# Kernel optimization log

Measured on AMD Instinct MI355X. Metric: run time of the kernel, lower is better.

## Reference

```python
import jax, jax.numpy as jnp
import numpy as np

MARGIN = 0.5        # contrastive margin (init kwarg)
NUM_LABELS = 20     # label ids are in [0, NUM_LABELS)


def setup_inputs() -> dict:
    key = jax.random.key(0)
    k1, k2 = jax.random.split(key)
    emb = jax.random.normal(k1, (4, 16, 64, 64), dtype=jnp.float32)
    lab = jax.random.randint(k2, (4, 64, 64), 0, NUM_LABELS, dtype=jnp.int32)
    return {"emb": emb, "lab": lab}


def _loss_one(x, y):
    # x: (C, H, W) embedding, y: (H, W) int labels
    C, H, W = x.shape
    N = H * W
    xf = x.reshape(C, N)
    # per-pixel centering across channels, then L2-normalize across channels
    xc = xf - jnp.mean(xf, axis=0, keepdims=True)
    nrm = jnp.sqrt(jnp.sum(xc * xc, axis=0))           # (N,)
    denom = jnp.where(nrm > 0, nrm, 1.0)
    e = jnp.where(nrm > 0, xc / denom, 0.0).T          # (N, C); NaN-mask -> 0
    sim = (e @ e.T) * 0.5 + 0.5                        # (N, N) in [0, 1]

    yi = y.reshape(N)
    yf = yi.astype(jnp.float32) + 1.0
    eq = yf[:, None] == yf[None, :]
    nz = (yf[:, None] * yf[None, :]) != 0.0            # product-zero exclusion (faithful)
    lp = jnp.where(nz, jnp.where(eq, 1.0, -1.0), 0.0)  # label-pair matrix

    # inverse-frequency per-pixel weights, outer product for pairs
    cnt = jnp.zeros((NUM_LABELS,), jnp.float32).at[yi].add(1.0)
    wpix = 1.0 / cnt[yi]                               # (N,)
    Wm = wpix[:, None] * wpix[None, :]                 # (N, N)

    # positive pairs: relu(1 - sim); negative pairs: relu(sim - margin)
    loss = jnp.where(lp == 1.0, jnp.maximum(1.0 - sim, 0.0),
                     jnp.where(lp == -1.0, jnp.maximum(sim - MARGIN, 0.0), 0.0))
    return jnp.sum(Wm * loss) / N


def reference(emb, lab):
    return jnp.sum(jax.vmap(_loss_one)(emb, lab))
```

## Files before the change

kernel.cpp:

```cpp
#include <hip/hip_runtime.h>

#define NUM_LABELS 20
#define N_PIX 4096
#define C_DIM 16
#define BATCH 4

#define PTILE 128
#define PNT (N_PIX / PTILE)
#define PTPAIRS (PNT * (PNT + 1) / 2)
#define NPAIRS (BATCH * PTPAIRS)
#define NBLK 704
#define BLK_PER_BATCH 176
#define KPAD 24

typedef __attribute__((ext_vector_type(8))) short bf16x8;
typedef __attribute__((ext_vector_type(4))) float f32x4;

__device__ __forceinline__ unsigned int bf16rne(float f) {
    unsigned int x = __float_as_uint(f);
    return (x + 0x7fffu + ((x >> 16) & 1u)) >> 16;
}

__global__ __launch_bounds__(256) void pair_kernel(
    const float* __restrict__ emb,
    const int*   __restrict__ lab,
    float* __restrict__ partials)
{
    const int bk   = blockIdx.x;
    const int b    = bk / BLK_PER_BATCH;
    const int t    = threadIdx.x;
    const int lane = t & 63;
    const int wv   = t >> 6;

    __shared__ int   h[NUM_LABELS];
    __shared__ float rinv[NUM_LABELS];
    __shared__ unsigned short sI[PTILE * KPAD];
    __shared__ unsigned short sJ[PTILE * KPAD];
    __shared__ int   syI[PTILE], syJ[PTILE];
    __shared__ float wred[4];

    if (t < NUM_LABELS) h[t] = 0;
    __syncthreads();
    {
        const int* yb = lab + (size_t)b * N_PIX;
        int cnt[NUM_LABELS];
#pragma unroll
        for (int l = 0; l < NUM_LABELS; ++l) cnt[l] = 0;
        for (int it = 0; it < 16; ++it) {
            const int y = yb[wv * 1024 + it * 64 + lane];
#pragma unroll
            for (int l = 0; l < NUM_LABELS; ++l)
                cnt[l] += (int)__popcll(__ballot(y == l));
        }
        if (lane == 0) {
#pragma unroll
            for (int l = 0; l < NUM_LABELS; ++l) atomicAdd(&h[l], cnt[l]);
        }
    }
    __syncthreads();
    if (t < NUM_LABELS) rinv[t] = (h[t] > 0) ? 1.0f / (float)h[t] : 0.0f;
    __syncthreads();

    float sum = 0.f;
    if ((bk % BLK_PER_BATCH) == 0 && t == 0) {
        int p = 0;
#pragma unroll
        for (int l = 0; l < NUM_LABELS; ++l) p += (h[l] > 0) ? 1 : 0;
        sum += 0.5f * (float)p;
    }

    for (int pi = 0; pi < 3; ++pi) {
        const int k0 = 3 * bk - b * PTPAIRS + pi;

        const float nn = (float)PNT;
        int ti = (int)(((2.f * nn + 1.f) -
                        sqrtf((2.f * nn + 1.f) * (2.f * nn + 1.f) - 8.f * (float)k0)) * 0.5f);
        if (ti < 0) ti = 0;
        if (ti > PNT - 1) ti = PNT - 1;
        auto rowoff = [](int r) { return r * PNT - (r * (r - 1)) / 2; };
        while (ti > 0 && k0 < rowoff(ti)) --ti;
        while (ti < PNT - 1 && k0 >= rowoff(ti + 1)) ++ti;
        const int tj = ti + (k0 - rowoff(ti));
        const bool diag = (ti == tj);

        __syncthreads();

        {
            const int side = t >> 7;
            const int row  = t & 127;
            const int tile = side ? tj : ti;
            const float* xb = emb + (size_t)b * C_DIM * N_PIX + tile * PTILE + row;

            float v[C_DIM];
            float s = 0.f;
#pragma unroll
            for (int c = 0; c < C_DIM; ++c) { v[c] = xb[(size_t)c * N_PIX]; s += v[c]; }
            const float mean = s * (1.0f / C_DIM);
            float ss = 0.f;
#pragma unroll
            for (int c = 0; c < C_DIM; ++c) { v[c] -= mean; ss += v[c] * v[c]; }
            const float nrm = sqrtf(ss);
            const int   y   = lab[b * N_PIX + tile * PTILE + row];
            const float w   = rinv[y];
            const float inv = (nrm > 0.f) ? (w / nrm) : 0.f;

            unsigned int u[8];
#pragma unroll
            for (int k = 0; k < 8; ++k) {
                const unsigned int lo = bf16rne(v[2 * k] * inv);
                const unsigned int hi = bf16rne(v[2 * k + 1] * inv);
                u[k] = lo | (hi << 16);
            }
            unsigned short* dst = side ? sJ : sI;
            *reinterpret_cast<uint4*>(&dst[row * KPAD])     = make_uint4(u[0], u[1], u[2], u[3]);
            *reinterpret_cast<uint4*>(&dst[row * KPAD + 8]) = make_uint4(u[4], u[5], u[6], u[7]);
            (side ? syJ : syI)[row] = y;

            if (diag && side == 0) sum -= 0.5f * (inv * inv * ss);
        }
        __syncthreads();

        const int lo16 = lane & 15;
        const int hi   = lane >> 4;
        const bool doread = (hi < 2);

        bf16x8 afrag[2] = {bf16x8{}, bf16x8{}};
        int    yIr[2][4];
#pragma unroll
        for (int rt = 0; rt < 2; ++rt) {
            const int rtile = wv * 2 + rt;
            if (doread)
                afrag[rt] = *reinterpret_cast<const bf16x8*>(&sI[(rtile * 16 + lo16) * KPAD + hi * 8]);
            const int4 yv = *reinterpret_cast<const int4*>(&syI[rtile * 16 + hi * 4]);
            yIr[rt][0] = yv.x; yIr[rt][1] = yv.y; yIr[rt][2] = yv.z; yIr[rt][3] = yv.w;
        }

#pragma unroll
        for (int ct = 0; ct < 8; ++ct) {
            bf16x8 bfrag = bf16x8{};
            if (doread)
                bfrag = *reinterpret_cast<const bf16x8*>(&sJ[(ct * 16 + lo16) * KPAD + hi * 8]);
            const int yq = syJ[ct * 16 + lo16];
#pragma unroll
            for (int rt = 0; rt < 2; ++rt) {
                const int rtile = wv * 2 + rt;
                if (diag && rtile > ct) continue;
                f32x4 acc = {0.f, 0.f, 0.f, 0.f};
                acc = __builtin_amdgcn_mfma_f32_16x16x32_bf16(afrag[rt], bfrag, acc, 0, 0, 0);
                if (diag && rtile == ct) {
#pragma unroll
                    for (int j = 0; j < 4; ++j) {
                        const float s = acc[j];
                        const float v = (yIr[rt][j] == yq) ? -s : fmaxf(s, 0.f);
                        const int iloc = hi * 4 + j;
                        sum += (iloc < lo16) ? v : 0.f;
                    }
                } else {
#pragma unroll
                    for (int j = 0; j < 4; ++j) {
                        const float s = acc[j];
                        sum += (yIr[rt][j] == yq) ? -s : fmaxf(s, 0.f);
                    }
                }
            }
        }
    }

#pragma unroll
    for (int off = 32; off > 0; off >>= 1) sum += __shfl_down(sum, off);
    if (lane == 0) wred[wv] = sum;
    __syncthreads();
    if (t == 0) partials[bk] = wred[0] + wred[1] + wred[2] + wred[3];
}

__global__ __launch_bounds__(256) void reduce_kernel(
    const float* __restrict__ partials, float* __restrict__ out)
{
    __shared__ double sd[256];
    const int t = threadIdx.x;
    double s = 0.0;
    for (int i = t; i < NBLK; i += 256) s += (double)partials[i];
    sd[t] = s;
    __syncthreads();
#pragma unroll
    for (int k = 128; k > 0; k >>= 1) {
        if (t < k) sd[t] += sd[t + k];
        __syncthreads();
    }
    if (t == 0) out[0] = (float)(sd[0] * (1.0 / (double)N_PIX));
}

extern "C" void kernel_launch(void* const* d_in, const int* in_sizes, int n_in,
                              void* d_out, int out_size, void* d_ws, size_t ws_size,
                              hipStream_t stream) {
    const float* emb = (const float*)d_in[0];
    const int*   lab = (const int*)d_in[1];
    float* out = (float*)d_out;
    float* partials = (float*)d_ws;

    pair_kernel<<<NBLK, 256, 0, stream>>>(emb, lab, partials);
    reduce_kernel<<<1, 256, 0, stream>>>(partials, out);
}
```

Before: 26.76 us.

## Precompute normalized bf16 embeddings in a prep kernel, pair kernel reads from global

```diff
diff --git a/kernel.cpp b/kernel.cpp
--- a/kernel.cpp
+++ b/kernel.cpp
@@ -9,9 +9,10 @@
 #define PNT (N_PIX / PTILE)
 #define PTPAIRS (PNT * (PNT + 1) / 2)
 #define NPAIRS (BATCH * PTPAIRS)
-#define NBLK 704
-#define BLK_PER_BATCH 176
-#define KPAD 24
+
+#define PREP_SLICES 16
+#define NPREP (BATCH * PREP_SLICES)
+#define NPART (NPREP + NPAIRS)
 
 typedef __attribute__((ext_vector_type(8))) short bf16x8;
 typedef __attribute__((ext_vector_type(4))) float f32x4;
@@ -21,26 +22,26 @@
     return (x + 0x7fffu + ((x >> 16) & 1u)) >> 16;
 }
 
-__global__ __launch_bounds__(256) void pair_kernel(
+__global__ __launch_bounds__(256) void prep_kernel(
     const float* __restrict__ emb,
     const int*   __restrict__ lab,
-    float* __restrict__ partials)
+    unsigned short* __restrict__ gT,
+    float* __restrict__ part)
 {
-    const int bk   = blockIdx.x;
-    const int b    = bk / BLK_PER_BATCH;
+    const int blk  = blockIdx.x;
+    const int b    = blk / PREP_SLICES;
+    const int sl   = blk % PREP_SLICES;
     const int t    = threadIdx.x;
+    const int wv   = t >> 6;
     const int lane = t & 63;
-    const int wv   = t >> 6;
 
     __shared__ int   h[NUM_LABELS];
     __shared__ float rinv[NUM_LABELS];
-    __shared__ unsigned short sI[PTILE * KPAD];
-    __shared__ unsigned short sJ[PTILE * KPAD];
-    __shared__ int   syI[PTILE], syJ[PTILE];
-    __shared__ float wred[4];
+    __shared__ float wsum[4];
 
     if (t < NUM_LABELS) h[t] = 0;
     __syncthreads();
+
     {
         const int* yb = lab + (size_t)b * N_PIX;
         int cnt[NUM_LABELS];
@@ -61,106 +62,117 @@
     if (t < NUM_LABELS) rinv[t] = (h[t] > 0) ? 1.0f / (float)h[t] : 0.0f;
     __syncthreads();
 
+    const int n = sl * 256 + t;
+    const float* xb = emb + (size_t)b * C_DIM * N_PIX + n;
+    float v[C_DIM];
+    float s = 0.f;
+#pragma unroll
+    for (int c = 0; c < C_DIM; ++c) { v[c] = xb[(size_t)c * N_PIX]; s += v[c]; }
+    const float mean = s * (1.0f / C_DIM);
+    float ss = 0.f;
+#pragma unroll
+    for (int c = 0; c < C_DIM; ++c) { v[c] -= mean; ss += v[c] * v[c]; }
+    const float nrm = sqrtf(ss);
+    const float w   = rinv[lab[(size_t)b * N_PIX + n]];
+    const float inv = (nrm > 0.f) ? (w / nrm) : 0.f;
+
+    unsigned int u[8];
+#pragma unroll
+    for (int k = 0; k < 8; ++k) {
+        const unsigned int lo = bf16rne(v[2 * k] * inv);
+        const unsigned int hi = bf16rne(v[2 * k + 1] * inv);
+        u[k] = lo | (hi << 16);
+    }
+    unsigned int* gp = (unsigned int*)(gT + ((size_t)b * N_PIX + n) * C_DIM);
+    *reinterpret_cast<uint4*>(gp)     = make_uint4(u[0], u[1], u[2], u[3]);
+    *reinterpret_cast<uint4*>(gp + 4) = make_uint4(u[4], u[5], u[6], u[7]);
+
+    float sq = inv * inv * ss;
+#pragma unroll
+    for (int off = 32; off > 0; off >>= 1) sq += __shfl_down(sq, off);
+    if (lane == 0) wsum[wv] = sq;
+    __syncthreads();
+    if (t == 0) {
+        float e = -0.5f * (wsum[0] + wsum[1] + wsum[2] + wsum[3]);
+        if (sl == 0) {
+            int p = 0;
+#pragma unroll
+            for (int l = 0; l < NUM_LABELS; ++l) p += (h[l] > 0) ? 1 : 0;
+            e += 0.5f * (float)p;
+        }
+        part[blk] = e;
+    }
+}
+
+__global__ __launch_bounds__(256) void pair_kernel(
+    const unsigned short* __restrict__ gT,
+    const int*   __restrict__ lab,
+    float* __restrict__ part)
+{
+    const int p  = blockIdx.x;
+    const int b  = p / PTPAIRS;
+    const int k0 = p % PTPAIRS;
+
+    const float nn = (float)PNT;
+    int ti = (int)(((2.f * nn + 1.f) -
+                    sqrtf((2.f * nn + 1.f) * (2.f * nn + 1.f) - 8.f * (float)k0)) * 0.5f);
+    if (ti < 0) ti = 0;
+    if (ti > PNT - 1) ti = PNT - 1;
+    auto rowoff = [](int r) { return r * PNT - (r * (r - 1)) / 2; };
+    while (ti > 0 && k0 < rowoff(ti)) --ti;
+    while (ti < PNT - 1 && k0 >= rowoff(ti + 1)) ++ti;
+    const int tj = ti + (k0 - rowoff(ti));
+    const bool diag = (ti == tj);
+
+    const int t    = threadIdx.x;
+    const int wv   = t >> 6;
+    const int lane = t & 63;
+    const int lo16 = lane & 15;
+    const int hi   = lane >> 4;
+    const bool doread = (hi < 2);
+
+    const unsigned short* gb = gT + (size_t)b * N_PIX * C_DIM;
+    const int* lb = lab + (size_t)b * N_PIX;
+
+    bf16x8 afrag[2] = {bf16x8{}, bf16x8{}};
+    int    yIr[2][4];
+#pragma unroll
+    for (int rt = 0; rt < 2; ++rt) {
+        const int rtile = wv * 2 + rt;
+        const int arow  = ti * PTILE + rtile * 16 + lo16;
+        if (doread)
+            afrag[rt] = *reinterpret_cast<const bf16x8*>(gb + (size_t)arow * C_DIM + hi * 8);
+        const int4 yv = *reinterpret_cast<const int4*>(lb + ti * PTILE + rtile * 16 + hi * 4);
+        yIr[rt][0] = yv.x; yIr[rt][1] = yv.y; yIr[rt][2] = yv.z; yIr[rt][3] = yv.w;
+    }
+
     float sum = 0.f;
-    if ((bk % BLK_PER_BATCH) == 0 && t == 0) {
-        int p = 0;
-#pragma unroll
-        for (int l = 0; l < NUM_LABELS; ++l) p += (h[l] > 0) ? 1 : 0;
-        sum += 0.5f * (float)p;
-    }
-
-    for (int pi = 0; pi < 3; ++pi) {
-        const int k0 = 3 * bk - b * PTPAIRS + pi;
-
-        const float nn = (float)PNT;
-        int ti = (int)(((2.f * nn + 1.f) -
-                        sqrtf((2.f * nn + 1.f) * (2.f * nn + 1.f) - 8.f * (float)k0)) * 0.5f);
-        if (ti < 0) ti = 0;
-        if (ti > PNT - 1) ti = PNT - 1;
-        auto rowoff = [](int r) { return r * PNT - (r * (r - 1)) / 2; };
-        while (ti > 0 && k0 < rowoff(ti)) --ti;
-        while (ti < PNT - 1 && k0 >= rowoff(ti + 1)) ++ti;
-        const int tj = ti + (k0 - rowoff(ti));
-        const bool diag = (ti == tj);
-
-        __syncthreads();
-
-        {
-            const int side = t >> 7;
-            const int row  = t & 127;
-            const int tile = side ? tj : ti;
-            const float* xb = emb + (size_t)b * C_DIM * N_PIX + tile * PTILE + row;
-
-            float v[C_DIM];
-            float s = 0.f;
-#pragma unroll
-            for (int c = 0; c < C_DIM; ++c) { v[c] = xb[(size_t)c * N_PIX]; s += v[c]; }
-            const float mean = s * (1.0f / C_DIM);
-            float ss = 0.f;
-#pragma unroll
-            for (int c = 0; c < C_DIM; ++c) { v[c] -= mean; ss += v[c] * v[c]; }
-            const float nrm = sqrtf(ss);
-            const int   y   = lab[b * N_PIX + tile * PTILE + row];
-            const float w   = rinv[y];
-            const float inv = (nrm > 0.f) ? (w / nrm) : 0.f;
-
-            unsigned int u[8];
-#pragma unroll
-            for (int k = 0; k < 8; ++k) {
-                const unsigned int lo = bf16rne(v[2 * k] * inv);
-                const unsigned int hi = bf16rne(v[2 * k + 1] * inv);
-                u[k] = lo | (hi << 16);
-            }
-            unsigned short* dst = side ? sJ : sI;
-            *reinterpret_cast<uint4*>(&dst[row * KPAD])     = make_uint4(u[0], u[1], u[2], u[3]);
-            *reinterpret_cast<uint4*>(&dst[row * KPAD + 8]) = make_uint4(u[4], u[5], u[6], u[7]);
-            (side ? syJ : syI)[row] = y;
-
-            if (diag && side == 0) sum -= 0.5f * (inv * inv * ss);
-        }
-        __syncthreads();
-
-        const int lo16 = lane & 15;
-        const int hi   = lane >> 4;
-        const bool doread = (hi < 2);
-
-        bf16x8 afrag[2] = {bf16x8{}, bf16x8{}};
-        int    yIr[2][4];
+#pragma unroll
+    for (int ct = 0; ct < 8; ++ct) {
+        const int brow = tj * PTILE + ct * 16 + lo16;
+        bf16x8 bfrag = bf16x8{};
+        if (doread)
+            bfrag = *reinterpret_cast<const bf16x8*>(gb + (size_t)brow * C_DIM + hi * 8);
+        const int yq = lb[tj * PTILE + ct * 16 + lo16];
 #pragma unroll
         for (int rt = 0; rt < 2; ++rt) {
             const int rtile = wv * 2 + rt;
-            if (doread)
-                afrag[rt] = *reinterpret_cast<const bf16x8*>(&sI[(rtile * 16 + lo16) * KPAD + hi * 8]);
-            const int4 yv = *reinterpret_cast<const int4*>(&syI[rtile * 16 + hi * 4]);
-            yIr[rt][0] = yv.x; yIr[rt][1] = yv.y; yIr[rt][2] = yv.z; yIr[rt][3] = yv.w;
-        }
-
-#pragma unroll
-        for (int ct = 0; ct < 8; ++ct) {
-            bf16x8 bfrag = bf16x8{};
-            if (doread)
-                bfrag = *reinterpret_cast<const bf16x8*>(&sJ[(ct * 16 + lo16) * KPAD + hi * 8]);
-            const int yq = syJ[ct * 16 + lo16];
-#pragma unroll
-            for (int rt = 0; rt < 2; ++rt) {
-                const int rtile = wv * 2 + rt;
-                if (diag && rtile > ct) continue;
-                f32x4 acc = {0.f, 0.f, 0.f, 0.f};
-                acc = __builtin_amdgcn_mfma_f32_16x16x32_bf16(afrag[rt], bfrag, acc, 0, 0, 0);
-                if (diag && rtile == ct) {
-#pragma unroll
-                    for (int j = 0; j < 4; ++j) {
-                        const float s = acc[j];
-                        const float v = (yIr[rt][j] == yq) ? -s : fmaxf(s, 0.f);
-                        const int iloc = hi * 4 + j;
-                        sum += (iloc < lo16) ? v : 0.f;
-                    }
-                } else {
-#pragma unroll
-                    for (int j = 0; j < 4; ++j) {
-                        const float s = acc[j];
-                        sum += (yIr[rt][j] == yq) ? -s : fmaxf(s, 0.f);
-                    }
+            if (diag && rtile > ct) continue;
+            f32x4 acc = {0.f, 0.f, 0.f, 0.f};
+            acc = __builtin_amdgcn_mfma_f32_16x16x32_bf16(afrag[rt], bfrag, acc, 0, 0, 0);
+            if (diag && rtile == ct) {
+#pragma unroll
+                for (int j = 0; j < 4; ++j) {
+                    const float s = acc[j];
+                    const float v = (yIr[rt][j] == yq) ? -s : fmaxf(s, 0.f);
+                    const int iloc = hi * 4 + j;
+                    sum += (iloc < lo16) ? v : 0.f;
+                }
+            } else {
+#pragma unroll
+                for (int j = 0; j < 4; ++j) {
+                    const float s = acc[j];
+                    sum += (yIr[rt][j] == yq) ? -s : fmaxf(s, 0.f);
                 }
             }
         }
@@ -168,18 +180,19 @@
 
 #pragma unroll
     for (int off = 32; off > 0; off >>= 1) sum += __shfl_down(sum, off);
+    __shared__ float wred[4];
     if (lane == 0) wred[wv] = sum;
     __syncthreads();
-    if (t == 0) partials[bk] = wred[0] + wred[1] + wred[2] + wred[3];
+    if (t == 0) part[NPREP + p] = wred[0] + wred[1] + wred[2] + wred[3];
 }
 
 __global__ __launch_bounds__(256) void reduce_kernel(
-    const float* __restrict__ partials, float* __restrict__ out)
+    const float* __restrict__ part, float* __restrict__ out)
 {
     __shared__ double sd[256];
     const int t = threadIdx.x;
     double s = 0.0;
-    for (int i = t; i < NBLK; i += 256) s += (double)partials[i];
+    for (int i = t; i < NPART; i += 256) s += (double)part[i];
     sd[t] = s;
     __syncthreads();
 #pragma unroll
@@ -196,8 +209,11 @@
     const float* emb = (const float*)d_in[0];
     const int*   lab = (const int*)d_in[1];
     float* out = (float*)d_out;
-    float* partials = (float*)d_ws;
-
-    pair_kernel<<<NBLK, 256, 0, stream>>>(emb, lab, partials);
-    reduce_kernel<<<1, 256, 0, stream>>>(partials, out);
-}
+
+    unsigned short* gT = (unsigned short*)d_ws;
+    float* part = (float*)(gT + (size_t)BATCH * N_PIX * C_DIM);
+
+    prep_kernel<<<NPREP, 256, 0, stream>>>(emb, lab, gT, part);
+    pair_kernel<<<NPAIRS, 256, 0, stream>>>(gT, lab, part);
+    reduce_kernel<<<1, 256, 0, stream>>>(part, out);
+}
```

Measured after the change: 26.04 us. -2.7%, faster.
